# Performance work log

Hardware: AMD Instinct MI355X
Metric: run time of the kernel (lower is better)

## Reference

```python
import jax, jax.numpy as jnp
import numpy as np

BETA = 0.001  # commitment loss weight from __init__ default


def setup_inputs() -> dict:
    key = jax.random.key(0)
    k1, k2 = jax.random.split(key)
    N, INPUT_DIM = 8192, 1024
    S, K, D = 32, 1024, 32  # nsplits, num_embeddings, embedding_dim
    z = jax.random.normal(k1, (N, INPUT_DIM), dtype=jnp.float32)
    # Stacked codebook weights: one [K, D] embedding table per split.
    W = jax.random.normal(k2, (S, K, D), dtype=jnp.float32)
    return {"z": z, "W": W}


def reference(z, W):
    N, INPUT_DIM = z.shape
    S, K, D = W.shape
    zc = z.reshape(N, S, D)  # per-split chunks, matches torch.chunk(z, S, -1)
    # Squared euclidean distances ||z||^2 + ||w||^2 - 2 z.w  -> [N, S, K]
    d2 = (
        jnp.sum(zc * zc, axis=-1, keepdims=True)
        + jnp.sum(W * W, axis=-1)[None, :, :]
        - 2.0 * jnp.einsum("nsd,skd->nsk", zc, W)
    )
    idx = jnp.argmin(d2, axis=-1)  # [N, S]
    # Gather nearest codes: W[s, idx[n, s]] -> [N, S, D]
    zq = W[jnp.arange(S)[None, :], idx]
    # Sum over splits of per-split mse means; equal split sizes so this is
    # S * mean over the whole tensor.
    sg = jax.lax.stop_gradient
    loss = S * (
        jnp.mean((sg(zq) - zc) ** 2) + BETA * jnp.mean((zq - sg(zc)) ** 2)
    )
    # Straight-through estimator
    zq_st = zc + sg(zq - zc)
    return zq_st.reshape(N, INPUT_DIM), loss
```

## Files before the change

kernel.cpp:

```cpp
#include <hip/hip_runtime.h>
#include <math.h>

#define NN 8192
#define SS 32
#define DD 32
#define KK 1024
#define OUT_ELEMS ((size_t)NN * SS * DD)

#define LOSS_SCALE (32.0f * 1.001f / 8388608.0f)

typedef _Float16 half8 __attribute__((ext_vector_type(8)));
typedef float   floatx4 __attribute__((ext_vector_type(4)));

#define CH_TILES 4
#define CHUNK_K  (CH_TILES * 16)
#define NCHUNK   (KK / CHUNK_K)
#define RG 2
#define NBLOCKS ((NN / 128) * SS)


__global__ __launch_bounds__(256, 4) void vq_fused(const float* __restrict__ z,
                                                   const float* __restrict__ W,
                                                   float* __restrict__ out,
                                                   float* __restrict__ part) {
    __shared__ _Float16 bufH[2][CH_TILES][64][8];
    __shared__ _Float16 bufL[2][CH_TILES][64][8];
    __shared__ float    w2b[2][CHUNK_K];
    __shared__ int      lds_idx[4][32];
    __shared__ float    lds_part[4];

    const int s    = blockIdx.x & (SS - 1);
    const int n0b  = (blockIdx.x >> 5) * 128;
    const int tid  = threadIdx.x;
    const int wv   = tid >> 6;
    const int lane = tid & 63;
    const int col  = lane & 15;
    const int quad = lane >> 4;

    const float* __restrict__ Ws = W + (size_t)s * KK * DD;
    const int n0w = n0b + wv * 32;

    half8 zh[RG], zl[RG];
    #pragma unroll
    for (int rg = 0; rg < RG; ++rg) {
        const float* zp = z + (size_t)(n0w + rg * 16 + col) * (SS * DD) + s * DD + quad * 8;
        const float4 va = ((const float4*)zp)[0];
        const float4 vb = ((const float4*)zp)[1];
        const float src[8] = {va.x, va.y, va.z, va.w, vb.x, vb.y, vb.z, vb.w};
        #pragma unroll
        for (int j = 0; j < 8; ++j) {
            const float v = -2.0f * src[j];
            const _Float16 h = (_Float16)v;
            zh[rg][j] = h;
            zl[rg][j] = (_Float16)(v - (float)h);
        }
    }

    const float* __restrict__ stg = Ws + ((size_t)(wv * 16 + col)) * DD + quad * 8;

    floatx4 best[RG];
    int bi[RG][4];
    #pragma unroll
    for (int rg = 0; rg < RG; ++rg) {
        best[rg] = (floatx4){INFINITY, INFINITY, INFINITY, INFINITY};
        bi[rg][0] = bi[rg][1] = bi[rg][2] = bi[rg][3] = 0;
    }

    float4 pa = ((const float4*)stg)[0];
    float4 pb = ((const float4*)stg)[1];
    {
        const float src[8] = {pa.x, pa.y, pa.z, pa.w, pb.x, pb.y, pb.z, pb.w};
        half8 h8, l8; float ps = 0.0f;
        #pragma unroll
        for (int j = 0; j < 8; ++j) {
            const float v = src[j];
            ps = fmaf(v, v, ps);
            const _Float16 h = (_Float16)v;
            h8[j] = h;
            l8[j] = (_Float16)(v - (float)h);
        }
        ps += __shfl_xor(ps, 16, 64);
        ps += __shfl_xor(ps, 32, 64);
        *(half8*)&bufH[0][wv][lane][0] = h8;
        *(half8*)&bufL[0][wv][lane][0] = l8;
        if (quad == 0) w2b[0][wv * 16 + col] = ps;
    }
    __syncthreads();

    for (int c = 0; c < NCHUNK; ++c) {
        const int b = c & 1;
        if (c + 1 < NCHUNK) {
            const float* nsrc = stg + (size_t)(c + 1) * CHUNK_K * DD;
            pa = ((const float4*)nsrc)[0];
            pb = ((const float4*)nsrc)[1];
        }

        #pragma unroll
        for (int tt = 0; tt < CH_TILES; ++tt) {
            const half8 bh = *(const half8*)&bufH[b][tt][lane][0];
            const half8 bl = *(const half8*)&bufL[b][tt][lane][0];
            const float wv2 = w2b[b][tt * 16 + col];
            const floatx4 c0 = {wv2, wv2, wv2, wv2};
            const int tk = c * CH_TILES + tt;
            #pragma unroll
            for (int rg = 0; rg < RG; ++rg) {
                floatx4 acc = __builtin_amdgcn_mfma_f32_16x16x32_f16(zh[rg], bh, c0, 0, 0, 0);
                acc = __builtin_amdgcn_mfma_f32_16x16x32_f16(zl[rg], bh, acc, 0, 0, 0);
                acc = __builtin_amdgcn_mfma_f32_16x16x32_f16(zh[rg], bl, acc, 0, 0, 0);
                #pragma unroll
                for (int i = 0; i < 4; ++i) {
                    if (acc[i] < best[rg][i]) { best[rg][i] = acc[i]; bi[rg][i] = tk; }
                }
            }
        }

        if (c + 1 < NCHUNK) {
            const float src[8] = {pa.x, pa.y, pa.z, pa.w, pb.x, pb.y, pb.z, pb.w};
            half8 h8, l8; float ps = 0.0f;
            #pragma unroll
            for (int j = 0; j < 8; ++j) {
                const float v = src[j];
                ps = fmaf(v, v, ps);
                const _Float16 h = (_Float16)v;
                h8[j] = h;
                l8[j] = (_Float16)(v - (float)h);
            }
            ps += __shfl_xor(ps, 16, 64);
            ps += __shfl_xor(ps, 32, 64);
            const int nb = (c + 1) & 1;
            *(half8*)&bufH[nb][wv][lane][0] = h8;
            *(half8*)&bufL[nb][wv][lane][0] = l8;
            if (quad == 0) w2b[nb][wv * 16 + col] = ps;
            __syncthreads();
        }
    }

    #pragma unroll
    for (int rg = 0; rg < RG; ++rg) {
        #pragma unroll
        for (int i = 0; i < 4; ++i) {
            float v = best[rg][i];
            int   k = bi[rg][i] * 16 + col;
            #pragma unroll
            for (int m = 1; m < 16; m <<= 1) {
                const float vo = __shfl_xor(v, m, 64);
                const int   ko = __shfl_xor(k, m, 64);
                if (vo < v || (vo == v && ko < k)) { v = vo; k = ko; }
            }
            if (col == 0) lds_idx[wv][rg * 16 + quad * 4 + i] = k;
        }
    }
    __syncthreads();

    const int r  = lane & 31;
    const int dh = (lane >> 5) * 16;
    const int krow = lds_idx[wv][r];
    const float* wsrc = Ws + (size_t)krow * DD + dh;
    const size_t zoff = (size_t)(n0w + r) * (SS * DD) + s * DD + dh;
    const float* zsrc = z + zoff;
    float* od = out + zoff;
    float sq = 0.0f;
    #pragma unroll
    for (int cc = 0; cc < 4; ++cc) {
        const float4 wq = ((const float4*)wsrc)[cc];
        const float4 zv = ((const float4*)zsrc)[cc];
        const float d0 = wq.x - zv.x, d1 = wq.y - zv.y;
        const float d2 = wq.z - zv.z, d3 = wq.w - zv.w;
        sq = fmaf(d0, d0, sq); sq = fmaf(d1, d1, sq);
        sq = fmaf(d2, d2, sq); sq = fmaf(d3, d3, sq);
        ((float4*)od)[cc] = wq;
    }
    #pragma unroll
    for (int off = 32; off > 0; off >>= 1) sq += __shfl_down(sq, off, 64);

    if (lane == 0) lds_part[wv] = sq;
    __syncthreads();
    if (tid == 0)
        part[blockIdx.x] = lds_part[0] + lds_part[1] + lds_part[2] + lds_part[3];
}

__global__ __launch_bounds__(256) void vq_loss(const float* __restrict__ part,
                                               float* __restrict__ out) {
    __shared__ float l[4];
    const int tid = threadIdx.x;
    float sum = 0.0f;
    #pragma unroll
    for (int i = 0; i < NBLOCKS / 256; ++i) sum += part[tid + i * 256];
    #pragma unroll
    for (int off = 32; off > 0; off >>= 1) sum += __shfl_down(sum, off, 64);
    if ((tid & 63) == 0) l[tid >> 6] = sum;
    __syncthreads();
    if (tid == 0) out[OUT_ELEMS] = (l[0] + l[1] + l[2] + l[3]) * LOSS_SCALE;
}

extern "C" void kernel_launch(void* const* d_in, const int* in_sizes, int n_in,
                              void* d_out, int out_size, void* d_ws, size_t ws_size,
                              hipStream_t stream) {
    const float* z = (const float*)d_in[0];
    const float* W = (const float*)d_in[1];
    float* out  = (float*)d_out;
    float* part = (float*)d_ws;

    vq_fused<<<dim3(NBLOCKS), dim3(256), 0, stream>>>(z, W, out, part);
    vq_loss<<<dim3(1), dim3(256), 0, stream>>>(part, out);
}
```

Measured before the change: 148.0 us.

## Double rows per block, widen codebook chunks, and software-pipeline LDS tile loads

Each block now handles 256 rows (four 16-row groups per wave) and stages 128 codebook entries per chunk, halving the number of blocks and of chunk barriers. Each staged codebook tile is therefore reused across twice as many z rows, halving codebook reloads and fp16 conversion work per row. The inner loop prefetches the next tile's fragments from LDS, issues the MFMAs for all row groups back to back, and raises wave priority around them. In exchange, register use and LDS footprint grow, which may lower occupancy and leaves only 1024 blocks to spread over the device.

```diff
diff --git a/kernel.cpp b/kernel.cpp
--- a/kernel.cpp
+++ b/kernel.cpp
@@ -12,11 +12,11 @@
 typedef _Float16 half8 __attribute__((ext_vector_type(8)));
 typedef float   floatx4 __attribute__((ext_vector_type(4)));
 
-#define CH_TILES 4
+#define CH_TILES 8
 #define CHUNK_K  (CH_TILES * 16)
 #define NCHUNK   (KK / CHUNK_K)
-#define RG 2
-#define NBLOCKS ((NN / 128) * SS)
+#define RG 4
+#define NBLOCKS ((NN / 256) * SS)
 
 
 __global__ __launch_bounds__(256, 4) void vq_fused(const float* __restrict__ z,
@@ -26,11 +26,11 @@
     __shared__ _Float16 bufH[2][CH_TILES][64][8];
     __shared__ _Float16 bufL[2][CH_TILES][64][8];
     __shared__ float    w2b[2][CHUNK_K];
-    __shared__ int      lds_idx[4][32];
+    __shared__ int      lds_idx[4][64];
     __shared__ float    lds_part[4];
 
     const int s    = blockIdx.x & (SS - 1);
-    const int n0b  = (blockIdx.x >> 5) * 128;
+    const int n0b  = (blockIdx.x >> 5) * 256;
     const int tid  = threadIdx.x;
     const int wv   = tid >> 6;
     const int lane = tid & 63;
@@ -38,7 +38,7 @@
     const int quad = lane >> 4;
 
     const float* __restrict__ Ws = W + (size_t)s * KK * DD;
-    const int n0w = n0b + wv * 32;
+    const int n0w = n0b + wv * 64;
 
     half8 zh[RG], zl[RG];
     #pragma unroll
@@ -66,10 +66,8 @@
         bi[rg][0] = bi[rg][1] = bi[rg][2] = bi[rg][3] = 0;
     }
 
-    float4 pa = ((const float4*)stg)[0];
-    float4 pb = ((const float4*)stg)[1];
-    {
-        const float src[8] = {pa.x, pa.y, pa.z, pa.w, pb.x, pb.y, pb.z, pb.w};
+    auto cvt_store = [&](const float4& va, const float4& vb, int nb, int tile) {
+        const float src[8] = {va.x, va.y, va.z, va.w, vb.x, vb.y, vb.z, vb.w};
         half8 h8, l8; float ps = 0.0f;
         #pragma unroll
         for (int j = 0; j < 8; ++j) {
@@ -81,10 +79,17 @@
         }
         ps += __shfl_xor(ps, 16, 64);
         ps += __shfl_xor(ps, 32, 64);
-        *(half8*)&bufH[0][wv][lane][0] = h8;
-        *(half8*)&bufL[0][wv][lane][0] = l8;
-        if (quad == 0) w2b[0][wv * 16 + col] = ps;
-    }
+        *(half8*)&bufH[nb][tile][lane][0] = h8;
+        *(half8*)&bufL[nb][tile][lane][0] = l8;
+        if (quad == 0) w2b[nb][tile * 16 + col] = ps;
+    };
+
+    float4 pa = ((const float4*)stg)[0];
+    float4 pb = ((const float4*)stg)[1];
+    float4 pc = ((const float4*)(stg + 64 * DD))[0];
+    float4 pd = ((const float4*)(stg + 64 * DD))[1];
+    cvt_store(pa, pb, 0, wv);
+    cvt_store(pc, pd, 0, 4 + wv);
     __syncthreads();
 
     for (int c = 0; c < NCHUNK; ++c) {
@@ -93,44 +98,52 @@
             const float* nsrc = stg + (size_t)(c + 1) * CHUNK_K * DD;
             pa = ((const float4*)nsrc)[0];
             pb = ((const float4*)nsrc)[1];
-        }
+            pc = ((const float4*)(nsrc + 64 * DD))[0];
+            pd = ((const float4*)(nsrc + 64 * DD))[1];
+        }
+
+        half8 bh0 = *(const half8*)&bufH[b][0][lane][0];
+        half8 bl0 = *(const half8*)&bufL[b][0][lane][0];
+        float w20 = w2b[b][col];
 
         #pragma unroll
         for (int tt = 0; tt < CH_TILES; ++tt) {
-            const half8 bh = *(const half8*)&bufH[b][tt][lane][0];
-            const half8 bl = *(const half8*)&bufL[b][tt][lane][0];
-            const float wv2 = w2b[b][tt * 16 + col];
-            const floatx4 c0 = {wv2, wv2, wv2, wv2};
+            half8 nbh, nbl; float nw2 = 0.0f;
+            if (tt + 1 < CH_TILES) {
+                nbh = *(const half8*)&bufH[b][tt + 1][lane][0];
+                nbl = *(const half8*)&bufL[b][tt + 1][lane][0];
+                nw2 = w2b[b][(tt + 1) * 16 + col];
+            }
+            const floatx4 c0 = {w20, w20, w20, w20};
             const int tk = c * CH_TILES + tt;
+
+            floatx4 acc[RG];
+            __builtin_amdgcn_s_setprio(1);
+            #pragma unroll
+            for (int rg = 0; rg < RG; ++rg)
+                acc[rg] = __builtin_amdgcn_mfma_f32_16x16x32_f16(zh[rg], bh0, c0, 0, 0, 0);
+            #pragma unroll
+            for (int rg = 0; rg < RG; ++rg)
+                acc[rg] = __builtin_amdgcn_mfma_f32_16x16x32_f16(zl[rg], bh0, acc[rg], 0, 0, 0);
+            #pragma unroll
+            for (int rg = 0; rg < RG; ++rg)
+                acc[rg] = __builtin_amdgcn_mfma_f32_16x16x32_f16(zh[rg], bl0, acc[rg], 0, 0, 0);
+            __builtin_amdgcn_s_setprio(0);
+
             #pragma unroll
             for (int rg = 0; rg < RG; ++rg) {
-                floatx4 acc = __builtin_amdgcn_mfma_f32_16x16x32_f16(zh[rg], bh, c0, 0, 0, 0);
-                acc = __builtin_amdgcn_mfma_f32_16x16x32_f16(zl[rg], bh, acc, 0, 0, 0);
-                acc = __builtin_amdgcn_mfma_f32_16x16x32_f16(zh[rg], bl, acc, 0, 0, 0);
                 #pragma unroll
                 for (int i = 0; i < 4; ++i) {
-                    if (acc[i] < best[rg][i]) { best[rg][i] = acc[i]; bi[rg][i] = tk; }
+                    if (acc[rg][i] < best[rg][i]) { best[rg][i] = acc[rg][i]; bi[rg][i] = tk; }
                 }
             }
+            bh0 = nbh; bl0 = nbl; w20 = nw2;
         }
 
         if (c + 1 < NCHUNK) {
-            const float src[8] = {pa.x, pa.y, pa.z, pa.w, pb.x, pb.y, pb.z, pb.w};
-            half8 h8, l8; float ps = 0.0f;
-            #pragma unroll
-            for (int j = 0; j < 8; ++j) {
-                const float v = src[j];
-                ps = fmaf(v, v, ps);
-                const _Float16 h = (_Float16)v;
-                h8[j] = h;
-                l8[j] = (_Float16)(v - (float)h);
-            }
-            ps += __shfl_xor(ps, 16, 64);
-            ps += __shfl_xor(ps, 32, 64);
             const int nb = (c + 1) & 1;
-            *(half8*)&bufH[nb][wv][lane][0] = h8;
-            *(half8*)&bufL[nb][wv][lane][0] = l8;
-            if (quad == 0) w2b[nb][wv * 16 + col] = ps;
+            cvt_store(pa, pb, nb, wv);
+            cvt_store(pc, pd, nb, 4 + wv);
             __syncthreads();
         }
     }
@@ -152,16 +165,14 @@
     }
     __syncthreads();
 
-    const int r  = lane & 31;
-    const int dh = (lane >> 5) * 16;
-    const int krow = lds_idx[wv][r];
-    const float* wsrc = Ws + (size_t)krow * DD + dh;
-    const size_t zoff = (size_t)(n0w + r) * (SS * DD) + s * DD + dh;
+    const int krow = lds_idx[wv][lane];
+    const float* wsrc = Ws + (size_t)krow * DD;
+    const size_t zoff = (size_t)(n0w + lane) * (SS * DD) + s * DD;
     const float* zsrc = z + zoff;
     float* od = out + zoff;
     float sq = 0.0f;
     #pragma unroll
-    for (int cc = 0; cc < 4; ++cc) {
+    for (int cc = 0; cc < 8; ++cc) {
         const float4 wq = ((const float4*)wsrc)[cc];
         const float4 zv = ((const float4*)zsrc)[cc];
         const float d0 = wq.x - zv.x, d1 = wq.y - zv.y;
```

New measurement: 410.8 us. 2.78x slower.

## Precompute split-fp16 codebook once and stream it via global_load_lds

Applied to the files above, without the earlier changes.

Adds a pre-pass kernel that converts W into hi/lo fp16 fragments and per-code squared norms in workspace, run once per call instead of in every block. The main kernel then stages these fragments straight into LDS with global_load_lds. Blocks grow to 8 waves with 128-wide K chunks, and the MFMA chain is interleaved across row groups under raised wave priority, with LDS reads prefetched one tile ahead. The change targets the redundant per-block conversion ALU work and the register round-trip of the staging path. In exchange it adds an extra kernel launch, extra workspace traffic, and a larger block footprint.

```diff
diff --git a/kernel.cpp b/kernel.cpp
--- a/kernel.cpp
+++ b/kernel.cpp
@@ -12,25 +12,75 @@
 typedef _Float16 half8 __attribute__((ext_vector_type(8)));
 typedef float   floatx4 __attribute__((ext_vector_type(4)));
 
-#define CH_TILES 4
+#define CH_TILES 8
 #define CHUNK_K  (CH_TILES * 16)
 #define NCHUNK   (KK / CHUNK_K)
 #define RG 2
-#define NBLOCKS ((NN / 128) * SS)
-
-
-__global__ __launch_bounds__(256, 4) void vq_fused(const float* __restrict__ z,
+#define WAVES 8
+#define BLK_ROWS (WAVES * RG * 16)
+#define NBLOCKS ((NN / BLK_ROWS) * SS)
+
+
+#define W2P_OFF  4096
+#define WHP_OFF  (W2P_OFF + SS * KK * 4)
+#define WLP_OFF  (WHP_OFF + SS * KK * DD * 2)
+
+typedef const __attribute__((address_space(1))) void* gas_p;
+typedef __attribute__((address_space(3))) void* las_p;
+
+__device__ __forceinline__ void gll16(const void* g, void* l) {
+    __builtin_amdgcn_global_load_lds((gas_p)g, (las_p)l, 16, 0, 0);
+}
+__device__ __forceinline__ void gll4(const void* g, void* l) {
+    __builtin_amdgcn_global_load_lds((gas_p)g, (las_p)l, 4, 0, 0);
+}
+
+__global__ __launch_bounds__(256) void w_pre(const float* __restrict__ W,
+                                             _Float16* __restrict__ WhP,
+                                             _Float16* __restrict__ WlP,
+                                             float* __restrict__ w2P) {
+    const int u    = blockIdx.x * 256 + threadIdx.x;
+    const int s    = u >> 12;
+    const int g    = (u >> 6) & 63;
+    const int l    = u & 63;
+    const int col  = l & 15;
+    const int quad = l >> 4;
+    const int k    = g * 16 + col;
+    const float* src = W + ((size_t)s * KK + k) * DD + quad * 8;
+    const float4 va = ((const float4*)src)[0];
+    const float4 vb = ((const float4*)src)[1];
+    const float v[8] = {va.x, va.y, va.z, va.w, vb.x, vb.y, vb.z, vb.w};
+    half8 h8, l8; float ps = 0.0f;
+    #pragma unroll
+    for (int j = 0; j < 8; ++j) {
+        const float x = v[j];
+        ps = fmaf(x, x, ps);
+        const _Float16 h = (_Float16)x;
+        h8[j] = h;
+        l8[j] = (_Float16)(x - (float)h);
+    }
+    ps += __shfl_xor(ps, 16, 64);
+    ps += __shfl_xor(ps, 32, 64);
+    *(half8*)(WhP + (size_t)u * 8) = h8;
+    *(half8*)(WlP + (size_t)u * 8) = l8;
+    if (quad == 0) w2P[s * KK + k] = ps;
+}
+
+__global__ __launch_bounds__(512, 4) void vq_fused(const float* __restrict__ z,
                                                    const float* __restrict__ W,
+                                                   const _Float16* __restrict__ WhP,
+                                                   const _Float16* __restrict__ WlP,
+                                                   const float* __restrict__ w2P,
                                                    float* __restrict__ out,
                                                    float* __restrict__ part) {
     __shared__ _Float16 bufH[2][CH_TILES][64][8];
     __shared__ _Float16 bufL[2][CH_TILES][64][8];
     __shared__ float    w2b[2][CHUNK_K];
-    __shared__ int      lds_idx[4][32];
-    __shared__ float    lds_part[4];
+    __shared__ int      lds_idx[WAVES][32];
+    __shared__ float    lds_part[WAVES];
 
     const int s    = blockIdx.x & (SS - 1);
-    const int n0b  = (blockIdx.x >> 5) * 128;
+    const int n0b  = (blockIdx.x >> 5) * BLK_ROWS;
     const int tid  = threadIdx.x;
     const int wv   = tid >> 6;
     const int lane = tid & 63;
@@ -38,7 +88,7 @@
     const int quad = lane >> 4;
 
     const float* __restrict__ Ws = W + (size_t)s * KK * DD;
-    const int n0w = n0b + wv * 32;
+    const int n0w = n0b + wv * (RG * 16);
 
     half8 zh[RG], zl[RG];
     #pragma unroll
@@ -56,8 +106,6 @@
         }
     }
 
-    const float* __restrict__ stg = Ws + ((size_t)(wv * 16 + col)) * DD + quad * 8;
-
     floatx4 best[RG];
     int bi[RG][4];
     #pragma unroll
@@ -66,73 +114,53 @@
         bi[rg][0] = bi[rg][1] = bi[rg][2] = bi[rg][3] = 0;
     }
 
-    float4 pa = ((const float4*)stg)[0];
-    float4 pb = ((const float4*)stg)[1];
-    {
-        const float src[8] = {pa.x, pa.y, pa.z, pa.w, pb.x, pb.y, pb.z, pb.w};
-        half8 h8, l8; float ps = 0.0f;
-        #pragma unroll
-        for (int j = 0; j < 8; ++j) {
-            const float v = src[j];
-            ps = fmaf(v, v, ps);
-            const _Float16 h = (_Float16)v;
-            h8[j] = h;
-            l8[j] = (_Float16)(v - (float)h);
-        }
-        ps += __shfl_xor(ps, 16, 64);
-        ps += __shfl_xor(ps, 32, 64);
-        *(half8*)&bufH[0][wv][lane][0] = h8;
-        *(half8*)&bufL[0][wv][lane][0] = l8;
-        if (quad == 0) w2b[0][wv * 16 + col] = ps;
-    }
+    const _Float16* whs = WhP + (size_t)s * 64 * 512 + (size_t)lane * 8;
+    const _Float16* wls = WlP + (size_t)s * 64 * 512 + (size_t)lane * 8;
+    const float*    w2s = w2P + (size_t)s * KK + lane;
+
+    auto stage = [&](int c, int nb) {
+        const size_t t = (size_t)c * CH_TILES + wv;
+        gll16(whs + t * 512, &bufH[nb][wv][0][0]);
+        gll16(wls + t * 512, &bufL[nb][wv][0][0]);
+        if (wv < 2) gll4(w2s + c * CHUNK_K + wv * 64, &w2b[nb][wv * 64]);
+    };
+
+    stage(0, 0);
     __syncthreads();
 
     for (int c = 0; c < NCHUNK; ++c) {
         const int b = c & 1;
-        if (c + 1 < NCHUNK) {
-            const float* nsrc = stg + (size_t)(c + 1) * CHUNK_K * DD;
-            pa = ((const float4*)nsrc)[0];
-            pb = ((const float4*)nsrc)[1];
+        if (c + 1 < NCHUNK) stage(c + 1, b ^ 1);
+
+        half8 bh = *(const half8*)&bufH[b][0][lane][0];
+        half8 bl = *(const half8*)&bufL[b][0][lane][0];
+        float w2v = w2b[b][col];
+        #pragma unroll
+        for (int tt = 0; tt < CH_TILES; ++tt) {
+            half8 nbh = bh, nbl = bl; float nw2 = w2v;
+            if (tt + 1 < CH_TILES) {
+                nbh = *(const half8*)&bufH[b][tt + 1][lane][0];
+                nbl = *(const half8*)&bufL[b][tt + 1][lane][0];
+                nw2 = w2b[b][(tt + 1) * 16 + col];
+            }
+            const floatx4 c0 = {w2v, w2v, w2v, w2v};
+            const int tk = c * CH_TILES + tt;
+            __builtin_amdgcn_s_setprio(1);
+            floatx4 a0 = __builtin_amdgcn_mfma_f32_16x16x32_f16(zh[0], bh, c0, 0, 0, 0);
+            floatx4 a1 = __builtin_amdgcn_mfma_f32_16x16x32_f16(zh[1], bh, c0, 0, 0, 0);
+            a0 = __builtin_amdgcn_mfma_f32_16x16x32_f16(zl[0], bh, a0, 0, 0, 0);
+            a1 = __builtin_amdgcn_mfma_f32_16x16x32_f16(zl[1], bh, a1, 0, 0, 0);
+            a0 = __builtin_amdgcn_mfma_f32_16x16x32_f16(zh[0], bl, a0, 0, 0, 0);
+            a1 = __builtin_amdgcn_mfma_f32_16x16x32_f16(zh[1], bl, a1, 0, 0, 0);
+            __builtin_amdgcn_s_setprio(0);
+            #pragma unroll
+            for (int i = 0; i < 4; ++i) {
+                if (a0[i] < best[0][i]) { best[0][i] = a0[i]; bi[0][i] = tk; }
+                if (a1[i] < best[1][i]) { best[1][i] = a1[i]; bi[1][i] = tk; }
+            }
+            bh = nbh; bl = nbl; w2v = nw2;
         }
-
-        #pragma unroll
-        for (int tt = 0; tt < CH_TILES; ++tt) {
-            const half8 bh = *(const half8*)&bufH[b][tt][lane][0];
-            const half8 bl = *(const half8*)&bufL[b][tt][lane][0];
-            const float wv2 = w2b[b][tt * 16 + col];
-            const floatx4 c0 = {wv2, wv2, wv2, wv2};
-            const int tk = c * CH_TILES + tt;
-            #pragma unroll
-            for (int rg = 0; rg < RG; ++rg) {
-                floatx4 acc = __builtin_amdgcn_mfma_f32_16x16x32_f16(zh[rg], bh, c0, 0, 0, 0);
-                acc = __builtin_amdgcn_mfma_f32_16x16x32_f16(zl[rg], bh, acc, 0, 0, 0);
-                acc = __builtin_amdgcn_mfma_f32_16x16x32_f16(zh[rg], bl, acc, 0, 0, 0);
-                #pragma unroll
-                for (int i = 0; i < 4; ++i) {
-                    if (acc[i] < best[rg][i]) { best[rg][i] = acc[i]; bi[rg][i] = tk; }
-                }
-            }
-        }
-
-        if (c + 1 < NCHUNK) {
-            const float src[8] = {pa.x, pa.y, pa.z, pa.w, pb.x, pb.y, pb.z, pb.w};
-            half8 h8, l8; float ps = 0.0f;
-            #pragma unroll
-            for (int j = 0; j < 8; ++j) {
-                const float v = src[j];
-                ps = fmaf(v, v, ps);
-                const _Float16 h = (_Float16)v;
-                h8[j] = h;
-                l8[j] = (_Float16)(v - (float)h);
-            }
-            ps += __shfl_xor(ps, 16, 64);
-            ps += __shfl_xor(ps, 32, 64);
-            const int nb = (c + 1) & 1;
-            *(half8*)&bufH[nb][wv][lane][0] = h8;
-            *(half8*)&bufL[nb][wv][lane][0] = l8;
-            if (quad == 0) w2b[nb][wv * 16 + col] = ps;
-            __syncthreads();
-        }
+        if (c + 1 < NCHUNK) __syncthreads();
     }
 
     #pragma unroll
@@ -175,8 +203,12 @@
 
     if (lane == 0) lds_part[wv] = sq;
     __syncthreads();
-    if (tid == 0)
-        part[blockIdx.x] = lds_part[0] + lds_part[1] + lds_part[2] + lds_part[3];
+    if (tid == 0) {
+        float t = 0.0f;
+        #pragma unroll
+        for (int w = 0; w < WAVES; ++w) t += lds_part[w];
+        part[blockIdx.x] = t;
+    }
 }
 
 __global__ __launch_bounds__(256) void vq_loss(const float* __restrict__ part,
@@ -199,8 +231,14 @@
     const float* z = (const float*)d_in[0];
     const float* W = (const float*)d_in[1];
     float* out  = (float*)d_out;
-    float* part = (float*)d_ws;
-
-    vq_fused<<<dim3(NBLOCKS), dim3(256), 0, stream>>>(z, W, out, part);
+
+    char* ws = (char*)d_ws;
+    float*    part = (float*)ws;
+    float*    w2P  = (float*)(ws + W2P_OFF);
+    _Float16* WhP  = (_Float16*)(ws + WHP_OFF);
+    _Float16* WlP  = (_Float16*)(ws + WLP_OFF);
+
+    w_pre<<<dim3(512), dim3(256), 0, stream>>>(W, WhP, WlP, w2P);
+    vq_fused<<<dim3(NBLOCKS), dim3(512), 0, stream>>>(z, W, WhP, WlP, w2P, out, part);
     vq_loss<<<dim3(1), dim3(256), 0, stream>>>(part, out);
 }
```

New measurement: 149.6 us. No clear change (+1.1%).
